# Kernel tuning notes

Hardware: AMD Instinct MI355X
Metric: run time of the kernel (lower is better)

Reference implementation:

```python
import jax, jax.numpy as jnp
import numpy as np

EMBED = 1024
HEADS = 16
HEAD_DIM = EMBED // HEADS


def setup_inputs() -> dict:
    key = jax.random.key(0)
    ks = jax.random.split(key, 6)
    B, T, C = 4, 2048, EMBED
    x = jax.random.normal(ks[0], (B, T, C), dtype=jnp.float32)
    # random binary mask [B,1,1,T]; keep at least one valid key per row by forcing first position to 1
    mask = jax.random.randint(ks[1], (B, 1, 1, T), 0, 2, dtype=jnp.int32)
    mask = mask.at[..., 0].set(1)
    scale = 1.0 / np.sqrt(C)
    qkv_w = jax.random.normal(ks[2], (3 * C, C), dtype=jnp.float32) * scale  # torch Linear weight [out,in]
    qkv_b = jax.random.normal(ks[3], (3 * C,), dtype=jnp.float32) * scale
    out_w = jax.random.normal(ks[4], (C, C), dtype=jnp.float32) * scale
    out_b = jax.random.normal(ks[5], (C,), dtype=jnp.float32) * scale
    return {"x": x, "mask": mask, "qkv_w": qkv_w, "qkv_b": qkv_b, "out_w": out_w, "out_b": out_b}


def reference(x, mask, qkv_w, qkv_b, out_w, out_b):
    B, T, C = x.shape
    H, D = HEADS, HEAD_DIM
    qkv = x @ qkv_w.T + qkv_b  # [B,T,3C]
    qkv = qkv.reshape(B, T, 3, H, D).transpose(2, 0, 3, 1, 4)  # [3,B,H,T,D]
    q, k, v = qkv[0], qkv[1], qkv[2]
    scores = jnp.einsum('bhqd,bhkd->bhqk', q, k) / np.sqrt(D)
    scores = jnp.where(mask == 0, -jnp.inf, scores)
    attn = jax.nn.softmax(scores, axis=-1)
    out = jnp.einsum('bhqk,bhkd->bhqd', attn, v)
    out = out.transpose(0, 2, 1, 3).reshape(B, T, C)
    return out @ out_w.T + out_b
```

## Files before the change

### kernel.cpp

```cpp
#include <hip/hip_runtime.h>
#include <hip/hip_bf16.h>

typedef _Float16 f16;
typedef _Float16 f16x4_t __attribute__((ext_vector_type(4)));
typedef _Float16 f16x8 __attribute__((ext_vector_type(8)));
typedef float f32x4 __attribute__((ext_vector_type(4)));

#define AS1(p) ((const __attribute__((address_space(1))) void*)(p))
#define AS3(p) ((__attribute__((address_space(3))) void*)(p))

__device__ __forceinline__ void gload_lds16(const f16* g, f16* l) {
    __builtin_amdgcn_global_load_lds(AS1(g), AS3(l), 16, 0, 0);
}

__device__ __forceinline__ f16x8 cvt8(float4 u, float4 v) {
    f16x8 r;
    r[0] = (f16)u.x; r[1] = (f16)u.y; r[2] = (f16)u.z; r[3] = (f16)u.w;
    r[4] = (f16)v.x; r[5] = (f16)v.y; r[6] = (f16)v.z; r[7] = (f16)v.w;
    return r;
}

#define Q_SCALE 0.180336880111f

__global__ __launch_bounds__(256) void pre_pass(
    const float* __restrict__ x, const float* __restrict__ qw,
    const int* __restrict__ mask, f16* __restrict__ x16,
    f16* __restrict__ w16, int* __restrict__ gpos, int* __restrict__ nkv)
{
    const int blk = blockIdx.x;
    if (blk >= 2048) {
        const int b = blk - 2048;
        if (threadIdx.x < 64) {
            const int lane = threadIdx.x;
            const int* mb = mask + b * 2048;
            int run = 0;
            for (int c = 0; c < 2048; c += 64) {
                int v = (mb[c + lane] != 0) ? 1 : 0;
                unsigned long long bits = __ballot(v);
                int pre = __popcll(bits & ((1ull << lane) - 1ull));
                if (v) gpos[b * 2048 + run + pre] = c + lane;
                run += __popcll(bits);
            }
            if (lane == 0) nkv[b] = run;
        }
        return;
    }
    const int nx8 = 8192 * 1024 / 8;
    const int nw8 = 3072 * 1024 / 8;
    int idx = blk * 256 + threadIdx.x;
    const int stride = 2048 * 256;
    for (int i = idx; i < nx8 + nw8; i += stride) {
        const float* s; f16* d;
        if (i < nx8) { size_t o = (size_t)i * 8;          s = x  + o; d = x16 + o; }
        else         { size_t o = (size_t)(i - nx8) * 8;  s = qw + o; d = w16 + o; }
        float4 u = *(const float4*)s;
        float4 v = *(const float4*)(s + 4);
        *(f16x8*)d = cvt8(u, v);
    }
}

__global__ __launch_bounds__(256) void cvt_f32_f16(
    const float* __restrict__ src, f16* __restrict__ dst, int n8)
{
    int idx = blockIdx.x * 256 + threadIdx.x;
    int stride = gridDim.x * 256;
    for (int i = idx; i < n8; i += stride) {
        size_t o = (size_t)i * 8;
        float4 u = *(const float4*)&src[o];
        float4 v = *(const float4*)&src[o + 4];
        *(f16x8*)&dst[o] = cvt8(u, v);
    }
}

__global__ __launch_bounds__(256) void gemm_qkv_f16(
    const f16* __restrict__ x16, const f16* __restrict__ w16,
    const float* __restrict__ bias, const int* __restrict__ gpos,
    const int* __restrict__ nkv, f16* __restrict__ q_g,
    f16* __restrict__ k_g, f16* __restrict__ vt_g)
{
    constexpr int BK = 64, K = 1024;
    __shared__ f16 As[128 * BK], Bs[128 * BK];

    const int tid  = threadIdx.x;
    const int lane = tid & 63, wave = tid >> 6;
    const int wy = wave >> 1, wx = wave & 1;
    const int lrow = lane & 15, quad = lane >> 4;
    const int srow = lane >> 3;
    const int sgrp = lane & 7;
    const int x0 = ((quad)     ^ (lrow & 7)) * 8;
    const int x1 = ((4 + quad) ^ (lrow & 7)) * 8;

    const int z  = blockIdx.z;
    const int bx = blockIdx.x, by = blockIdx.y;
    int b_kv = 0, mt = 0, nk = 0, nbase, n0;
    if (z == 0) {
        if (bx >= 8) return;
        nbase = 0; n0 = bx * 128;
    } else {
        b_kv = by >> 4; mt = by & 15;
        nk = nkv[b_kv];
        if (mt * 128 >= nk) return;
        nbase = 1024; n0 = bx * 128;
    }

    const f16* arow[4];
    const f16* brow[4];
#pragma unroll
    for (int j = 0; j < 4; ++j) {
        int rit = (wave * 4 + j) * 8 + srow;
        int trow;
        if (z == 0) {
            trow = by * 128 + rit;
        } else {
            int ct = mt * 128 + rit;
            int t = (ct < nk) ? gpos[b_kv * 2048 + ct] : 0;
            trow = b_kv * 2048 + t;
        }
        arow[j] = x16 + (size_t)trow * K + (sgrp ^ srow) * 8;
        brow[j] = w16 + (size_t)(nbase + n0 + rit) * K + (sgrp ^ srow) * 8;
    }

    f32x4 acc[4][4] = {};

    for (int k0 = 0; k0 < K; k0 += BK) {
        __syncthreads();
#pragma unroll
        for (int j = 0; j < 4; ++j) {
            int rg = wave * 4 + j;
            gload_lds16(arow[j] + k0, &As[rg * 512 + lane * 8]);
            gload_lds16(brow[j] + k0, &Bs[rg * 512 + lane * 8]);
        }
        __syncthreads();

        f16x8 a0[4], a1[4], b0[4], b1[4];
#pragma unroll
        for (int i = 0; i < 4; ++i) {
            const int r = (wy * 64 + i * 16 + lrow) * BK;
            a0[i] = *(const f16x8*)&As[r + x0];
            a1[i] = *(const f16x8*)&As[r + x1];
        }
#pragma unroll
        for (int j = 0; j < 4; ++j) {
            const int r = (wx * 64 + j * 16 + lrow) * BK;
            b0[j] = *(const f16x8*)&Bs[r + x0];
            b1[j] = *(const f16x8*)&Bs[r + x1];
        }
#pragma unroll
        for (int i = 0; i < 4; ++i)
#pragma unroll
            for (int j = 0; j < 4; ++j) {
                acc[i][j] = __builtin_amdgcn_mfma_f32_16x16x32_f16(a0[i], b0[j], acc[i][j], 0, 0, 0);
                acc[i][j] = __builtin_amdgcn_mfma_f32_16x16x32_f16(a1[i], b1[j], acc[i][j], 0, 0, 0);
            }
    }

    if (z == 0) {
#pragma unroll
        for (int i = 0; i < 4; ++i) {
            size_t row = (size_t)by * 128 + wy * 64 + i * 16 + quad * 4;
            int b = (int)(row >> 11);
            int t = (int)(row & 2047);
#pragma unroll
            for (int j = 0; j < 4; ++j) {
                int col = n0 + wx * 64 + j * 16 + lrow;
                float bb = bias[col];
                int hh = col >> 6, d = col & 63;
                size_t o = ((size_t)(b * 16 + hh) * 2048 + t) * 64 + d;
#pragma unroll
                for (int r = 0; r < 4; ++r)
                    q_g[o + (size_t)r * 64] = (f16)((acc[i][j][r] + bb) * Q_SCALE);
            }
        }
    } else {
        const int region = n0 >> 10;
#pragma unroll
        for (int i = 0; i < 4; ++i) {
            int ct = mt * 128 + wy * 64 + i * 16 + quad * 4;
#pragma unroll
            for (int j = 0; j < 4; ++j) {
                int col = n0 + wx * 64 + j * 16 + lrow;
                float bb = bias[1024 + col];
                int cl = col & 1023, hh = cl >> 6, d = cl & 63;
                size_t bh = (size_t)(b_kv * 16 + hh);
                if (region == 0) {
#pragma unroll
                    for (int r = 0; r < 4; ++r)
                        k_g[(bh * 2048 + ct + r) * 64 + d] = (f16)(acc[i][j][r] + bb);
                } else {
                    f16x4_t pv;
#pragma unroll
                    for (int r = 0; r < 4; ++r) pv[r] = (f16)(acc[i][j][r] + bb);
                    *(f16x4_t*)&vt_g[(bh * 64 + d) * 2048 + ct] = pv;
                }
            }
        }
    }
}

__global__ __launch_bounds__(256) void gemm2_f16(
    const f16* __restrict__ A16, const f16* __restrict__ Bw16,
    const float* __restrict__ bias, float* __restrict__ C,
    int M, int N, int K)
{
    constexpr int BK = 64;
    __shared__ f16 As[128 * BK], Bs[128 * BK];

    const int tid  = threadIdx.x;
    const int lane = tid & 63, wave = tid >> 6;
    const int wy = wave >> 1, wx = wave & 1;
    const int lrow = lane & 15, quad = lane >> 4;
    const size_t m0 = (size_t)blockIdx.y * 128;
    const size_t n0 = (size_t)blockIdx.x * 128;
    const int srow = lane >> 3, sgrp = lane & 7;
    const int x0 = ((quad)     ^ (lrow & 7)) * 8;
    const int x1 = ((4 + quad) ^ (lrow & 7)) * 8;

    f32x4 acc[4][4] = {};

    for (int k0 = 0; k0 < K; k0 += BK) {
        __syncthreads();
#pragma unroll
        for (int j = 0; j < 4; ++j) {
            int rg  = wave * 4 + j;
            int row = rg * 8 + srow;
            int grp = sgrp ^ srow;
            gload_lds16(&A16[(m0 + row) * (size_t)K + k0 + grp * 8],
                        &As[rg * 512 + lane * 8]);
            gload_lds16(&Bw16[(n0 + row) * (size_t)K + k0 + grp * 8],
                        &Bs[rg * 512 + lane * 8]);
        }
        __syncthreads();

        f16x8 a0[4], a1[4], b0[4], b1[4];
#pragma unroll
        for (int i = 0; i < 4; ++i) {
            const int r = (wy * 64 + i * 16 + lrow) * BK;
            a0[i] = *(const f16x8*)&As[r + x0];
            a1[i] = *(const f16x8*)&As[r + x1];
        }
#pragma unroll
        for (int j = 0; j < 4; ++j) {
            const int r = (wx * 64 + j * 16 + lrow) * BK;
            b0[j] = *(const f16x8*)&Bs[r + x0];
            b1[j] = *(const f16x8*)&Bs[r + x1];
        }
#pragma unroll
        for (int i = 0; i < 4; ++i)
#pragma unroll
            for (int j = 0; j < 4; ++j) {
                acc[i][j] = __builtin_amdgcn_mfma_f32_16x16x32_f16(a0[i], b0[j], acc[i][j], 0, 0, 0);
                acc[i][j] = __builtin_amdgcn_mfma_f32_16x16x32_f16(a1[i], b1[j], acc[i][j], 0, 0, 0);
            }
    }

#pragma unroll
    for (int i = 0; i < 4; ++i) {
        size_t row = m0 + wy * 64 + i * 16 + quad * 4;
#pragma unroll
        for (int j = 0; j < 4; ++j) {
            size_t col = n0 + wx * 64 + j * 16 + lrow;
            float bb = bias[col];
#pragma unroll
            for (int r = 0; r < 4; ++r)
                C[(row + r) * N + col] = acc[i][j][r] + bb;
        }
    }
}

__global__ __launch_bounds__(256) void attn_f16(
    const f16* __restrict__ q_g, const f16* __restrict__ k_g,
    const f16* __restrict__ vt_g, const int* __restrict__ nkv,
    f16* __restrict__ att, int B, int T)
{
    constexpr int LDP = 72;
    __shared__ f16 Ks_s[2][64 * 64];
    __shared__ f16 Vt_s[2][64 * 64];
    __shared__ f16 Pt[128 * LDP];

    const int tid  = threadIdx.x;
    const int lane = tid & 63, wave = tid >> 6;
    const int lrow = lane & 15, quad = lane >> 4;
    const int bid = ((int)blockIdx.x & 7) * 128 + ((int)blockIdx.x >> 3);
    const int qt = bid & 15;
    const int h  = (bid >> 4) & 15;
    const int b  = bid >> 8;
    const size_t base = (size_t)b * T;
    const size_t bh = (size_t)(b * 16 + h);
    const f16* qg_base = q_g  + bh * (2048 * 64);
    const f16* kg_base = k_g  + bh * (2048 * 64);
    const f16* vt_base = vt_g + bh * (64 * 2048);

    const int nk = nkv[b];
    const int ntiles = (nk + 63) >> 6;

    const int x0 = ((quad)     ^ (lrow & 7)) * 8;
    const int x1 = ((4 + quad) ^ (lrow & 7)) * 8;

    f16x8 aq[2][2];
#pragma unroll
    for (int qi = 0; qi < 2; ++qi)
#pragma unroll
        for (int ks = 0; ks < 2; ++ks)
            aq[qi][ks] = *(const f16x8*)&qg_base[
                (size_t)(qt * 128 + wave * 32 + qi * 16 + lrow) * 64 + ks * 32 + quad * 8];

    f32x4 oacc[2][4] = {};
    float l_part[2] = {0.f, 0.f};

    const int srow0 = (lane >> 3);
    const int sgrp  = (lane & 7);

    auto stage = [&](int kt, int bsel) {
        const f16* kT = kg_base + kt * 4096;
#pragma unroll
        for (int j = 0; j < 2; ++j) {
            int rg  = wave + j * 4;
            int row = rg * 8 + srow0;
            int grp = sgrp ^ (row & 7);
            gload_lds16(&kT[row * 64 + grp * 8], &Ks_s[bsel][rg * 512 + lane * 8]);
            gload_lds16(&vt_base[(size_t)row * 2048 + kt * 64 + grp * 8],
                        &Vt_s[bsel][rg * 512 + lane * 8]);
        }
    };

    stage(0, 0);
    __syncthreads();

    for (int kt = 0; kt < ntiles; ++kt) {
        const int cur = kt & 1;
        if (kt + 1 < ntiles) stage(kt + 1, cur ^ 1);

        const f16* Ks = Ks_s[cur];
        const f16* Vt = Vt_s[cur];

        f32x4 s[2][4];
        __builtin_amdgcn_s_setprio(1);
#pragma unroll
        for (int ni = 0; ni < 4; ++ni) {
            const int key = ni * 16 + lrow;
            f16x8 k0 = *(const f16x8*)&Ks[key * 64 + x0];
            f16x8 k1 = *(const f16x8*)&Ks[key * 64 + x1];
#pragma unroll
            for (int qi = 0; qi < 2; ++qi) {
                f32x4 t = {0.f, 0.f, 0.f, 0.f};
                t = __builtin_amdgcn_mfma_f32_16x16x32_f16(k0, aq[qi][0], t, 0, 0, 0);
                t = __builtin_amdgcn_mfma_f32_16x16x32_f16(k1, aq[qi][1], t, 0, 0, 0);
                s[qi][ni] = t;
            }
        }
        __builtin_amdgcn_s_setprio(0);

        const int rem = nk - kt * 64;
        auto softmax = [&](bool masked) {
#pragma unroll
            for (int qi = 0; qi < 2; ++qi)
#pragma unroll
                for (int ni = 0; ni < 4; ++ni) {
                    float p[4];
#pragma unroll
                    for (int r = 0; r < 4; ++r) {
                        float e = __builtin_amdgcn_exp2f(s[qi][ni][r]);
                        p[r] = (!masked || (ni * 16 + quad * 4 + r) < rem) ? e : 0.f;
                    }
                    l_part[qi] += (p[0] + p[1]) + (p[2] + p[3]);
                    f16x4_t pk;
#pragma unroll
                    for (int r = 0; r < 4; ++r) pk[r] = (f16)p[r];
                    *(f16x4_t*)&Pt[(wave * 32 + qi * 16 + lrow) * LDP + ni * 16 + quad * 4] = pk;
                }
        };
        if (rem >= 64) softmax(false); else softmax(true);

        f16x8 pf[2][2];
#pragma unroll
        for (int qi = 0; qi < 2; ++qi)
#pragma unroll
            for (int ks = 0; ks < 2; ++ks)
                pf[qi][ks] = *(const f16x8*)&Pt[(wave * 32 + qi * 16 + lrow) * LDP + ks * 32 + quad * 8];
        __builtin_amdgcn_s_setprio(1);
#pragma unroll
        for (int di = 0; di < 4; ++di) {
            const int d = di * 16 + lrow;
            f16x8 v0 = *(const f16x8*)&Vt[d * 64 + x0];
            f16x8 v1 = *(const f16x8*)&Vt[d * 64 + x1];
#pragma unroll
            for (int qi = 0; qi < 2; ++qi) {
                oacc[qi][di] = __builtin_amdgcn_mfma_f32_16x16x32_f16(v0, pf[qi][0], oacc[qi][di], 0, 0, 0);
                oacc[qi][di] = __builtin_amdgcn_mfma_f32_16x16x32_f16(v1, pf[qi][1], oacc[qi][di], 0, 0, 0);
            }
        }
        __builtin_amdgcn_s_setprio(0);

        __syncthreads();
    }

#pragma unroll
    for (int qi = 0; qi < 2; ++qi) {
        float v = l_part[qi];
        v += __shfl_xor(v, 16);
        v += __shfl_xor(v, 32);
        float inv = 1.f / v;
        int q = qt * 128 + wave * 32 + qi * 16 + lrow;
#pragma unroll
        for (int di = 0; di < 4; ++di) {
            f16x4_t o;
#pragma unroll
            for (int r = 0; r < 4; ++r) o[r] = (f16)(oacc[qi][di][r] * inv);
            *(f16x4_t*)&att[(base + q) * 1024 + h * 64 + di * 16 + quad * 4] = o;
        }
    }
}

extern "C" void kernel_launch(void* const* d_in, const int* in_sizes, int n_in,
                              void* d_out, int out_size, void* d_ws, size_t ws_size,
                              hipStream_t stream) {
    const float* x     = (const float*)d_in[0];
    const int*   mask  = (const int*)d_in[1];
    const float* qkv_w = (const float*)d_in[2];
    const float* qkv_b = (const float*)d_in[3];
    const float* out_w = (const float*)d_in[4];
    const float* out_b = (const float*)d_in[5];
    float* out = (float*)d_out;

    const int B = 4, T = 2048;
    const int M = B * T;
    char* ws = (char*)d_ws;
    f16* q_g = (f16*)(ws);
    f16* k_g = (f16*)(ws + 16777216);
    f16* vt  = (f16*)(ws + 33554432);
    f16* att = (f16*)(ws + 50331648);

    f16* x16 = (f16*)d_out;
    f16* w16 = (f16*)((char*)d_out + 16777216);
    int* gpos = (int*)((char*)d_out + 23068672);
    int* nkv  = gpos + 4 * 2048;
    f16* ow16 = q_g;

    dim3 blk(256);
    pre_pass<<<dim3(2052), blk, 0, stream>>>(x, qkv_w, mask, x16, w16, gpos, nkv);
    gemm_qkv_f16<<<dim3(16, 64, 2), blk, 0, stream>>>(x16, w16, qkv_b, gpos, nkv, q_g, k_g, vt);
    attn_f16<<<dim3(B * 16 * 16), blk, 0, stream>>>(q_g, k_g, vt, nkv, att, B, T);
    cvt_f32_f16<<<dim3(512), blk, 0, stream>>>(out_w, ow16, 1024 * 1024 / 8);
    gemm2_f16<<<dim3(1024 / 128, M / 128), blk, 0, stream>>>(att, ow16, out_b, out, M, 1024, 1024);
}
```

Baseline: 272.4 us.

## Double-buffer LDS tiles in both GEMMs and flatten QKV grid

Both f16 GEMM kernels now use two LDS buffers, so the global-to-LDS load of the next K tile is issued before the MFMAs on the current tile, with one barrier per iteration instead of two. MFMA sections are wrapped in s_setprio raises. The QKV GEMM grid goes from a 3D launch with many early-exiting blocks to a 2D grid of 24 column tiles, where blocks with bx>=8 handle K/V. LDS use doubles to 64KB per block, which may reduce occupancy.

```diff
diff --git a/kernel.cpp b/kernel.cpp
--- a/kernel.cpp
+++ b/kernel.cpp
@@ -78,8 +78,8 @@
     const int* __restrict__ nkv, f16* __restrict__ q_g,
     f16* __restrict__ k_g, f16* __restrict__ vt_g)
 {
-    constexpr int BK = 64, K = 1024;
-    __shared__ f16 As[128 * BK], Bs[128 * BK];
+    constexpr int BK = 64, K = 1024, NT = K / BK;
+    __shared__ f16 As[2][128 * BK], Bs[2][128 * BK];
 
     const int tid  = threadIdx.x;
     const int lane = tid & 63, wave = tid >> 6;
@@ -90,17 +90,16 @@
     const int x0 = ((quad)     ^ (lrow & 7)) * 8;
     const int x1 = ((4 + quad) ^ (lrow & 7)) * 8;
 
-    const int z  = blockIdx.z;
     const int bx = blockIdx.x, by = blockIdx.y;
+    const int z = (bx >= 8);
     int b_kv = 0, mt = 0, nk = 0, nbase, n0;
-    if (z == 0) {
-        if (bx >= 8) return;
+    if (!z) {
         nbase = 0; n0 = bx * 128;
     } else {
         b_kv = by >> 4; mt = by & 15;
         nk = nkv[b_kv];
         if (mt * 128 >= nk) return;
-        nbase = 1024; n0 = bx * 128;
+        nbase = 1024; n0 = (bx - 8) * 128;
     }
 
     const f16* arow[4];
@@ -109,7 +108,7 @@
     for (int j = 0; j < 4; ++j) {
         int rit = (wave * 4 + j) * 8 + srow;
         int trow;
-        if (z == 0) {
+        if (!z) {
             trow = by * 128 + rit;
         } else {
             int ct = mt * 128 + rit;
@@ -120,31 +119,38 @@
         brow[j] = w16 + (size_t)(nbase + n0 + rit) * K + (sgrp ^ srow) * 8;
     }
 
-    f32x4 acc[4][4] = {};
-
-    for (int k0 = 0; k0 < K; k0 += BK) {
-        __syncthreads();
+    auto stage = [&](int k0, int bsel) {
 #pragma unroll
         for (int j = 0; j < 4; ++j) {
             int rg = wave * 4 + j;
-            gload_lds16(arow[j] + k0, &As[rg * 512 + lane * 8]);
-            gload_lds16(brow[j] + k0, &Bs[rg * 512 + lane * 8]);
-        }
-        __syncthreads();
+            gload_lds16(arow[j] + k0, &As[bsel][rg * 512 + lane * 8]);
+            gload_lds16(brow[j] + k0, &Bs[bsel][rg * 512 + lane * 8]);
+        }
+    };
+
+    f32x4 acc[4][4] = {};
+
+    stage(0, 0);
+    __syncthreads();
+
+    for (int kt = 0; kt < NT; ++kt) {
+        const int cur = kt & 1;
+        if (kt + 1 < NT) stage((kt + 1) * BK, cur ^ 1);
 
         f16x8 a0[4], a1[4], b0[4], b1[4];
 #pragma unroll
         for (int i = 0; i < 4; ++i) {
             const int r = (wy * 64 + i * 16 + lrow) * BK;
-            a0[i] = *(const f16x8*)&As[r + x0];
-            a1[i] = *(const f16x8*)&As[r + x1];
+            a0[i] = *(const f16x8*)&As[cur][r + x0];
+            a1[i] = *(const f16x8*)&As[cur][r + x1];
         }
 #pragma unroll
         for (int j = 0; j < 4; ++j) {
             const int r = (wx * 64 + j * 16 + lrow) * BK;
-            b0[j] = *(const f16x8*)&Bs[r + x0];
-            b1[j] = *(const f16x8*)&Bs[r + x1];
-        }
+            b0[j] = *(const f16x8*)&Bs[cur][r + x0];
+            b1[j] = *(const f16x8*)&Bs[cur][r + x1];
+        }
+        __builtin_amdgcn_s_setprio(1);
 #pragma unroll
         for (int i = 0; i < 4; ++i)
 #pragma unroll
@@ -152,9 +158,12 @@
                 acc[i][j] = __builtin_amdgcn_mfma_f32_16x16x32_f16(a0[i], b0[j], acc[i][j], 0, 0, 0);
                 acc[i][j] = __builtin_amdgcn_mfma_f32_16x16x32_f16(a1[i], b1[j], acc[i][j], 0, 0, 0);
             }
-    }
-
-    if (z == 0) {
+        __builtin_amdgcn_s_setprio(0);
+
+        __syncthreads();
+    }
+
+    if (!z) {
 #pragma unroll
         for (int i = 0; i < 4; ++i) {
             size_t row = (size_t)by * 128 + wy * 64 + i * 16 + quad * 4;
@@ -203,7 +212,7 @@
     int M, int N, int K)
 {
     constexpr int BK = 64;
-    __shared__ f16 As[128 * BK], Bs[128 * BK];
+    __shared__ f16 As[2][128 * BK], Bs[2][128 * BK];
 
     const int tid  = threadIdx.x;
     const int lane = tid & 63, wave = tid >> 6;
@@ -215,35 +224,48 @@
     const int x0 = ((quad)     ^ (lrow & 7)) * 8;
     const int x1 = ((4 + quad) ^ (lrow & 7)) * 8;
 
+    const f16* arow[4];
+    const f16* brow[4];
+#pragma unroll
+    for (int j = 0; j < 4; ++j) {
+        int rit = (wave * 4 + j) * 8 + srow;
+        arow[j] = A16  + (m0 + rit) * (size_t)K + (sgrp ^ srow) * 8;
+        brow[j] = Bw16 + (n0 + rit) * (size_t)K + (sgrp ^ srow) * 8;
+    }
+
+    auto stage = [&](int k0, int bsel) {
+#pragma unroll
+        for (int j = 0; j < 4; ++j) {
+            int rg = wave * 4 + j;
+            gload_lds16(arow[j] + k0, &As[bsel][rg * 512 + lane * 8]);
+            gload_lds16(brow[j] + k0, &Bs[bsel][rg * 512 + lane * 8]);
+        }
+    };
+
     f32x4 acc[4][4] = {};
-
-    for (int k0 = 0; k0 < K; k0 += BK) {
-        __syncthreads();
-#pragma unroll
-        for (int j = 0; j < 4; ++j) {
-            int rg  = wave * 4 + j;
-            int row = rg * 8 + srow;
-            int grp = sgrp ^ srow;
-            gload_lds16(&A16[(m0 + row) * (size_t)K + k0 + grp * 8],
-                        &As[rg * 512 + lane * 8]);
-            gload_lds16(&Bw16[(n0 + row) * (size_t)K + k0 + grp * 8],
-                        &Bs[rg * 512 + lane * 8]);
-        }
-        __syncthreads();
+    const int NT = K / BK;
+
+    stage(0, 0);
+    __syncthreads();
+
+    for (int kt = 0; kt < NT; ++kt) {
+        const int cur = kt & 1;
+        if (kt + 1 < NT) stage((kt + 1) * BK, cur ^ 1);
 
         f16x8 a0[4], a1[4], b0[4], b1[4];
 #pragma unroll
         for (int i = 0; i < 4; ++i) {
             const int r = (wy * 64 + i * 16 + lrow) * BK;
-            a0[i] = *(const f16x8*)&As[r + x0];
-            a1[i] = *(const f16x8*)&As[r + x1];
+            a0[i] = *(const f16x8*)&As[cur][r + x0];
+            a1[i] = *(const f16x8*)&As[cur][r + x1];
         }
 #pragma unroll
         for (int j = 0; j < 4; ++j) {
             const int r = (wx * 64 + j * 16 + lrow) * BK;
-            b0[j] = *(const f16x8*)&Bs[r + x0];
-            b1[j] = *(const f16x8*)&Bs[r + x1];
-        }
+            b0[j] = *(const f16x8*)&Bs[cur][r + x0];
+            b1[j] = *(const f16x8*)&Bs[cur][r + x1];
+        }
+        __builtin_amdgcn_s_setprio(1);
 #pragma unroll
         for (int i = 0; i < 4; ++i)
 #pragma unroll
@@ -251,6 +273,9 @@
                 acc[i][j] = __builtin_amdgcn_mfma_f32_16x16x32_f16(a0[i], b0[j], acc[i][j], 0, 0, 0);
                 acc[i][j] = __builtin_amdgcn_mfma_f32_16x16x32_f16(a1[i], b1[j], acc[i][j], 0, 0, 0);
             }
+        __builtin_amdgcn_s_setprio(0);
+
+        __syncthreads();
     }
 
 #pragma unroll
@@ -438,7 +463,7 @@
 
     dim3 blk(256);
     pre_pass<<<dim3(2052), blk, 0, stream>>>(x, qkv_w, mask, x16, w16, gpos, nkv);
-    gemm_qkv_f16<<<dim3(16, 64, 2), blk, 0, stream>>>(x16, w16, qkv_b, gpos, nkv, q_g, k_g, vt);
+    gemm_qkv_f16<<<dim3(24, 64), blk, 0, stream>>>(x16, w16, qkv_b, gpos, nkv, q_g, k_g, vt);
     attn_f16<<<dim3(B * 16 * 16), blk, 0, stream>>>(q_g, k_g, vt, nkv, att, B, T);
     cvt_f32_f16<<<dim3(512), blk, 0, stream>>>(out_w, ow16, 1024 * 1024 / 8);
     gemm2_f16<<<dim3(1024 / 128, M / 128), blk, 0, stream>>>(att, ow16, out_b, out, M, 1024, 1024);
```

After: 255.5 us. -6.2%, faster.
